# Performance work log

Hardware: AMD Instinct MI355X
Metric: run time of the kernel (lower is better)

Reference implementation:

```python
import jax, jax.numpy as jnp
import numpy as np

N_NODES = 50000
N_EDGES = 300000
D_IN = 256
D_HID = 256


def setup_inputs() -> dict:
    key = jax.random.key(0)
    ks = jax.random.split(key, 9)
    x = jax.random.normal(ks[0], (N_NODES, D_IN), dtype=jnp.float32)
    src = jax.random.randint(ks[1], (N_EDGES,), 0, N_NODES, dtype=jnp.int64)
    dst = jax.random.randint(ks[2], (N_EDGES,), 0, N_NODES, dtype=jnp.int64)
    # Kaiming-uniform-ish init like nn.Linear defaults
    def lin(k, fan_in, fan_out):
        bound = 1.0 / np.sqrt(fan_in)
        kw, kb = jax.random.split(k)
        W = jax.random.uniform(kw, (fan_out, fan_in), minval=-bound, maxval=bound, dtype=jnp.float32)
        b = jax.random.uniform(kb, (fan_out,), minval=-bound, maxval=bound, dtype=jnp.float32)
        return W, b
    W1, b1 = lin(ks[3], 2 * D_IN, D_HID)
    W2, b2 = lin(ks[4], D_HID, D_HID)
    W3, b3 = lin(ks[5], D_HID, 1)
    return {"x": x, "src": src, "dst": dst,
            "W1": W1, "b1": b1, "W2": W2, "b2": b2, "W3": W3, "b3": b3}


def reference(x, src, dst, W1, b1, W2, b2, W3, b3):
    # gather src/dst node features per edge and concat -> [E, 2*D_IN]
    h = jnp.concatenate([x[src], x[dst]], axis=1)
    h = jax.nn.relu(h @ W1.T + b1)          # [E, D_HID]
    h = jax.nn.relu(h @ W2.T + b2)          # dropout is identity in eval mode
    score = h @ W3.T + b3                   # [E, 1]
    return score
```

## Files before the change

kernel.cpp:

```cpp
#include <hip/hip_runtime.h>

typedef short bfx8 __attribute__((ext_vector_type(8)));
typedef float fx4 __attribute__((ext_vector_type(4)));

#define D 256
#define E_TILE 64

__device__ __forceinline__ float b2f(short s) {
  union { unsigned u; float f; } v; v.u = ((unsigned)(unsigned short)s) << 16; return v.f;
}
__device__ __forceinline__ short f2b(float f) {
  union { float f; unsigned u; } v; v.f = f;
  unsigned u = v.u;
  u += 0x7fffu + ((u >> 16) & 1u);
  return (short)(u >> 16);
}
__device__ __forceinline__ float relu(float f) { return f > 0.f ? f : 0.f; }

__global__ void k_prep(const float* __restrict__ W1, const float* __restrict__ W2,
                       unsigned short* __restrict__ B1, unsigned short* __restrict__ W2b) {
  int t = blockIdx.x * 256 + threadIdx.x;
  if (t < 512 * 256) {
    int n = t >> 8, k = t & 255;
    float v = (n < 256) ? W1[n * 512 + k] : W1[(n - 256) * 512 + 256 + k];
    B1[t] = (unsigned short)f2b(v);
  } else if (t < 512 * 256 + 256 * 256) {
    int i = t - 512 * 256;
    W2b[i] = (unsigned short)f2b(W2[i]);
  }
}

__launch_bounds__(256, 2)
__global__ void k_node(const float* __restrict__ x, const unsigned short* __restrict__ B1,
                       unsigned short* __restrict__ PQ, int n_nodes) {
  __shared__ __align__(16) short smA[64 * 40];
  __shared__ __align__(16) short smW[512 * 40];
  short* smT = smW;
  const int tid = threadIdx.x;
  const int wave = tid >> 6, lane = tid & 63;
  const int lr = lane & 15, lg = lane >> 4;
  const int m0 = blockIdx.x * 64;

  fx4 acc[4][8] = {};

#pragma unroll 1
  for (int ks = 0; ks < 8; ++ks) {
    const int k0 = ks * 32;
    {
      int r = tid >> 2, c = (tid & 3) * 8;
      int m = m0 + r;
      bfx8 o;
      if (m < n_nodes) {
        const float* p = x + (size_t)m * 256 + k0 + c;
        float4 v0 = *(const float4*)(p);
        float4 v1 = *(const float4*)(p + 4);
        o[0] = f2b(v0.x); o[1] = f2b(v0.y); o[2] = f2b(v0.z); o[3] = f2b(v0.w);
        o[4] = f2b(v1.x); o[5] = f2b(v1.y); o[6] = f2b(v1.z); o[7] = f2b(v1.w);
      } else {
        o = (bfx8){0,0,0,0,0,0,0,0};
      }
      *(bfx8*)&smA[r * 40 + c] = o;
    }
#pragma unroll
    for (int it = 0; it < 8; ++it) {
      int idx = it * 256 + tid;
      int n = idx >> 2, c = (idx & 3) * 8;
      bfx8 v = *(const bfx8*)(B1 + n * 256 + k0 + c);
      *(bfx8*)&smW[n * 40 + c] = v;
    }
    __syncthreads();
    bfx8 af[4];
#pragma unroll
    for (int mt = 0; mt < 4; ++mt)
      af[mt] = *(const bfx8*)&smA[(mt * 16 + lr) * 40 + lg * 8];
#pragma unroll
    for (int nt = 0; nt < 8; ++nt) {
      int n = wave * 128 + nt * 16 + lr;
      bfx8 bf = *(const bfx8*)&smW[n * 40 + lg * 8];
#pragma unroll
      for (int mt = 0; mt < 4; ++mt)
        acc[mt][nt] = __builtin_amdgcn_mfma_f32_16x16x32_bf16(af[mt], bf, acc[mt][nt], 0, 0, 0);
    }
    __syncthreads();
  }

#pragma unroll
  for (int h = 0; h < 2; ++h) {
#pragma unroll
    for (int mt2 = 0; mt2 < 2; ++mt2) {
      const int mt = 2 * h + mt2;
#pragma unroll
      for (int nt = 0; nt < 8; ++nt)
#pragma unroll
        for (int i = 0; i < 4; ++i) {
          int mrow = mt2 * 16 + lg * 4 + i;
          int n = wave * 128 + nt * 16 + lr;
          smT[mrow * 520 + n] = f2b(acc[mt][nt][i]);
        }
    }
    __syncthreads();
    int r = tid >> 3, cbase = (tid & 7) * 8;
    int m = m0 + h * 32 + r;
    if (m < n_nodes) {
#pragma unroll
      for (int j = 0; j < 8; ++j) {
        int c = cbase + j * 64;
        *(bfx8*)(PQ + (size_t)m * 512 + c) = *(const bfx8*)&smT[r * 520 + c];
      }
    }
    __syncthreads();
  }
}

__launch_bounds__(256, 2)
__global__ void k_edge(const unsigned short* __restrict__ PQ,
                       const int* __restrict__ src, const int* __restrict__ dst,
                       const float* __restrict__ b1, const unsigned short* __restrict__ W2b,
                       const float* __restrict__ b2, const float* __restrict__ W3,
                       const float* __restrict__ b3, float* __restrict__ out,
                       int E, int ntiles) {
  __shared__ __align__(16) short smH[64 * 264];
  __shared__ float smS[4][64];
  __shared__ float smB1[256];
  const int tid = threadIdx.x;
  const int wave = tid >> 6, lane = tid & 63;
  const int lr = lane & 15, lg = lane >> 4;

  if (tid < 256) smB1[tid] = b1[tid];

  bfx8 bw[4][8];
  float b2v[4], w3v[4];
#pragma unroll
  for (int nt = 0; nt < 4; ++nt) {
    int n = wave * 64 + nt * 16 + lr;
    b2v[nt] = b2[n];
    w3v[nt] = W3[n];
#pragma unroll
    for (int ks = 0; ks < 8; ++ks)
      bw[nt][ks] = *(const bfx8*)(W2b + n * 256 + ks * 32 + lg * 8);
  }
  const float b3v = b3[0];
  __syncthreads();

  for (int tile = blockIdx.x; tile < ntiles; tile += gridDim.x) {
    const int base = tile * E_TILE;
    {
      int r = tid >> 2;
      int e = base + r;
      if (e < E) {
        int s = src[e], d = dst[e];
        const unsigned short* ps = PQ + (size_t)s * 512;
        const unsigned short* pd = PQ + (size_t)d * 512 + 256;
#pragma unroll
        for (int it = 0; it < 8; ++it) {
          int c = (tid & 3) * 8 + it * 32;
          bfx8 pv = *(const bfx8*)(ps + c);
          bfx8 qv = *(const bfx8*)(pd + c);
          bfx8 o;
#pragma unroll
          for (int j = 0; j < 8; ++j)
            o[j] = f2b(relu(b2f(pv[j]) + b2f(qv[j]) + smB1[c + j]));
          *(bfx8*)&smH[r * 264 + c] = o;
        }
      } else {
        bfx8 z = (bfx8){0,0,0,0,0,0,0,0};
#pragma unroll
        for (int it = 0; it < 8; ++it) {
          int c = (tid & 3) * 8 + it * 32;
          *(bfx8*)&smH[r * 264 + c] = z;
        }
      }
    }
    __syncthreads();

    fx4 acc[4][4] = {};
#pragma unroll
    for (int ks = 0; ks < 8; ++ks) {
      bfx8 af[4];
#pragma unroll
      for (int mt = 0; mt < 4; ++mt)
        af[mt] = *(const bfx8*)&smH[(mt * 16 + lr) * 264 + ks * 32 + lg * 8];
#pragma unroll
      for (int nt = 0; nt < 4; ++nt)
#pragma unroll
        for (int mt = 0; mt < 4; ++mt)
          acc[mt][nt] = __builtin_amdgcn_mfma_f32_16x16x32_bf16(af[mt], bw[nt][ks], acc[mt][nt], 0, 0, 0);
    }

#pragma unroll
    for (int mt = 0; mt < 4; ++mt)
#pragma unroll
      for (int i = 0; i < 4; ++i) {
        float p = 0.f;
#pragma unroll
        for (int nt = 0; nt < 4; ++nt)
          p += relu(acc[mt][nt][i] + b2v[nt]) * w3v[nt];
        p += __shfl_xor(p, 1);
        p += __shfl_xor(p, 2);
        p += __shfl_xor(p, 4);
        p += __shfl_xor(p, 8);
        if (lr == 0) smS[wave][mt * 16 + lg * 4 + i] = p;
      }
    __syncthreads();
    if (tid < 64) {
      int e = base + tid;
      if (e < E) out[e] = smS[0][tid] + smS[1][tid] + smS[2][tid] + smS[3][tid] + b3v;
    }
    __syncthreads();
  }
}

__global__ void k_fallback(const float* __restrict__ x, const int* __restrict__ src,
                           const int* __restrict__ dst, const float* __restrict__ W1,
                           const float* __restrict__ b1, const float* __restrict__ W2,
                           const float* __restrict__ b2, const float* __restrict__ W3,
                           const float* __restrict__ b3, float* __restrict__ out, int E) {
  __shared__ float smF[4][512];
  __shared__ float smG[4][256];
  int wave = threadIdx.x >> 6, lane = threadIdx.x & 63;
  int e = blockIdx.x * 4 + wave;
  bool valid = e < E;
  int ec = valid ? e : 0;
  int s = src[ec], d = dst[ec];
  for (int j = 0; j < 8; ++j) {
    int k = lane * 8 + j;
    smF[wave][k] = (k < 256) ? x[(size_t)s * 256 + k] : x[(size_t)d * 256 + k - 256];
  }
  __syncthreads();
  for (int t = 0; t < 4; ++t) {
    int n = lane + t * 64;
    float a = b1[n];
    for (int k = 0; k < 512; ++k) a += smF[wave][k] * W1[n * 512 + k];
    smG[wave][n] = relu(a);
  }
  __syncthreads();
  float p = 0.f;
  for (int t = 0; t < 4; ++t) {
    int n = lane + t * 64;
    float a = b2[n];
    for (int k = 0; k < 256; ++k) a += smG[wave][k] * W2[n * 256 + k];
    p += relu(a) * W3[n];
  }
  for (int m = 1; m < 64; m <<= 1) p += __shfl_xor(p, m);
  if (lane == 0 && valid) out[e] = p + b3[0];
}

extern "C" void kernel_launch(void* const* d_in, const int* in_sizes, int n_in,
                              void* d_out, int out_size, void* d_ws, size_t ws_size,
                              hipStream_t stream) {
  const float* x  = (const float*)d_in[0];
  const int*   src = (const int*)d_in[1];
  const int*   dst = (const int*)d_in[2];
  const float* W1 = (const float*)d_in[3];
  const float* b1 = (const float*)d_in[4];
  const float* W2 = (const float*)d_in[5];
  const float* b2 = (const float*)d_in[6];
  const float* W3 = (const float*)d_in[7];
  const float* b3 = (const float*)d_in[8];
  float* out = (float*)d_out;

  const int E = in_sizes[1];
  const int n_nodes = in_sizes[0] / 256;

  const size_t offB1 = 0;
  const size_t offW2 = (size_t)512 * 256 * 2;
  const size_t offPQ = offW2 + (size_t)256 * 256 * 2;
  const size_t need = offPQ + (size_t)n_nodes * 512 * 2;

  if (ws_size >= need) {
    unsigned short* B1  = (unsigned short*)((char*)d_ws + offB1);
    unsigned short* W2b = (unsigned short*)((char*)d_ws + offW2);
    unsigned short* PQ  = (unsigned short*)((char*)d_ws + offPQ);
    k_prep<<<768, 256, 0, stream>>>(W1, W2, B1, W2b);
    k_node<<<(n_nodes + 63) / 64, 256, 0, stream>>>(x, B1, PQ, n_nodes);
    const int ntiles = (E + E_TILE - 1) / E_TILE;
    k_edge<<<1024, 256, 0, stream>>>(PQ, src, dst, b1, W2b, b2, W3, b3, out, E, ntiles);
  } else {
    k_fallback<<<(E + 3) / 4, 256, 0, stream>>>(x, src, dst, W1, b1, W2, b2, W3, b3, out, E);
  }
}
```

Measured before the change: 217.3 us.

## Prefetch next edge tile's gathers into registers and double-buffer shared memory

The edge kernel now issues the PQ gathers for the next tile into registers while the MFMA for the current tile runs, and alternates between two shared-memory H buffers, which removes one barrier per tile. The b1 bias is folded into the node-kernel output so the edge kernel no longer reads it from shared memory. The edge grid is halved to 512 blocks to make room for the extra registers and LDS, which raises register pressure and lowers occupancy. Per-edge bias addition before the bf16 rounding of PQ changes the rounding slightly.

After: 266.3 us. 1.23x slower.

```diff
diff --git a/kernel.cpp b/kernel.cpp
--- a/kernel.cpp
+++ b/kernel.cpp
@@ -32,6 +32,7 @@
 
 __launch_bounds__(256, 2)
 __global__ void k_node(const float* __restrict__ x, const unsigned short* __restrict__ B1,
+                       const float* __restrict__ b1,
                        unsigned short* __restrict__ PQ, int n_nodes) {
   __shared__ __align__(16) short smA[64 * 40];
   __shared__ __align__(16) short smW[512 * 40];
@@ -40,6 +41,13 @@
   const int wave = tid >> 6, lane = tid & 63;
   const int lr = lane & 15, lg = lane >> 4;
   const int m0 = blockIdx.x * 64;
+
+  float b1v[8];
+#pragma unroll
+  for (int nt = 0; nt < 8; ++nt) {
+    int n = wave * 128 + nt * 16 + lr;
+    b1v[nt] = (n < 256) ? b1[n] : 0.f;
+  }
 
   fx4 acc[4][8] = {};
 
@@ -95,7 +103,7 @@
         for (int i = 0; i < 4; ++i) {
           int mrow = mt2 * 16 + lg * 4 + i;
           int n = wave * 128 + nt * 16 + lr;
-          smT[mrow * 520 + n] = f2b(acc[mt][nt][i]);
+          smT[mrow * 520 + n] = f2b(acc[mt][nt][i] + b1v[nt]);
         }
     }
     __syncthreads();
@@ -115,18 +123,16 @@
 __launch_bounds__(256, 2)
 __global__ void k_edge(const unsigned short* __restrict__ PQ,
                        const int* __restrict__ src, const int* __restrict__ dst,
-                       const float* __restrict__ b1, const unsigned short* __restrict__ W2b,
+                       const unsigned short* __restrict__ W2b,
                        const float* __restrict__ b2, const float* __restrict__ W3,
                        const float* __restrict__ b3, float* __restrict__ out,
                        int E, int ntiles) {
-  __shared__ __align__(16) short smH[64 * 264];
+  __shared__ __align__(16) short smH[2 * 64 * 264];
   __shared__ float smS[4][64];
-  __shared__ float smB1[256];
   const int tid = threadIdx.x;
   const int wave = tid >> 6, lane = tid & 63;
   const int lr = lane & 15, lg = lane >> 4;
-
-  if (tid < 256) smB1[tid] = b1[tid];
+  const int G = gridDim.x;
 
   bfx8 bw[4][8];
   float b2v[4], w3v[4];
@@ -140,38 +146,54 @@
       bw[nt][ks] = *(const bfx8*)(W2b + n * 256 + ks * 32 + lg * 8);
   }
   const float b3v = b3[0];
-  __syncthreads();
-
-  for (int tile = blockIdx.x; tile < ntiles; tile += gridDim.x) {
-    const int base = tile * E_TILE;
-    {
-      int r = tid >> 2;
-      int e = base + r;
-      if (e < E) {
-        int s = src[e], d = dst[e];
-        const unsigned short* ps = PQ + (size_t)s * 512;
-        const unsigned short* pd = PQ + (size_t)d * 512 + 256;
-#pragma unroll
-        for (int it = 0; it < 8; ++it) {
-          int c = (tid & 3) * 8 + it * 32;
-          bfx8 pv = *(const bfx8*)(ps + c);
-          bfx8 qv = *(const bfx8*)(pd + c);
-          bfx8 o;
-#pragma unroll
-          for (int j = 0; j < 8; ++j)
-            o[j] = f2b(relu(b2f(pv[j]) + b2f(qv[j]) + smB1[c + j]));
-          *(bfx8*)&smH[r * 264 + c] = o;
-        }
-      } else {
-        bfx8 z = (bfx8){0,0,0,0,0,0,0,0};
-#pragma unroll
-        for (int it = 0; it < 8; ++it) {
-          int c = (tid & 3) * 8 + it * 32;
-          *(bfx8*)&smH[r * 264 + c] = z;
-        }
+
+  const int r = tid >> 2, cb = (tid & 3) * 8;
+  const int t0 = blockIdx.x;
+
+  bfx8 pv[8], qv[8];
+  int sN, dN;
+
+  {
+    int e = t0 * E_TILE + r; if (e >= E) e = 0;
+    int s0 = src[e], d0 = dst[e];
+    const unsigned short* ps = PQ + (size_t)s0 * 512;
+    const unsigned short* pd = PQ + (size_t)d0 * 512 + 256;
+#pragma unroll
+    for (int it = 0; it < 8; ++it) {
+      int c = cb + it * 32;
+      pv[it] = *(const bfx8*)(ps + c);
+      qv[it] = *(const bfx8*)(pd + c);
+    }
+    int e2 = (t0 + G) * E_TILE + r; if (e2 >= E) e2 = 0;
+    sN = src[e2]; dN = dst[e2];
+  }
+
+  int buf = 0;
+  for (int t = t0; t < ntiles; t += G) {
+    short* Hb = &smH[buf * (64 * 264)];
+#pragma unroll
+    for (int it = 0; it < 8; ++it) {
+      int c = cb + it * 32;
+      bfx8 o;
+#pragma unroll
+      for (int j = 0; j < 8; ++j)
+        o[j] = f2b(relu(b2f(pv[it][j]) + b2f(qv[it][j])));
+      *(bfx8*)&Hb[r * 264 + c] = o;
+    }
+    __syncthreads();
+
+    if (t + G < ntiles) {
+      const unsigned short* ps = PQ + (size_t)sN * 512;
+      const unsigned short* pd = PQ + (size_t)dN * 512 + 256;
+#pragma unroll
+      for (int it = 0; it < 8; ++it) {
+        int c = cb + it * 32;
+        pv[it] = *(const bfx8*)(ps + c);
+        qv[it] = *(const bfx8*)(pd + c);
       }
-    }
-    __syncthreads();
+      int e2 = (t + 2 * G) * E_TILE + r; if (e2 >= E) e2 = 0;
+      sN = src[e2]; dN = dst[e2];
+    }
 
     fx4 acc[4][4] = {};
 #pragma unroll
@@ -179,7 +201,7 @@
       bfx8 af[4];
 #pragma unroll
       for (int mt = 0; mt < 4; ++mt)
-        af[mt] = *(const bfx8*)&smH[(mt * 16 + lr) * 264 + ks * 32 + lg * 8];
+        af[mt] = *(const bfx8*)&Hb[(mt * 16 + lr) * 264 + ks * 32 + lg * 8];
 #pragma unroll
       for (int nt = 0; nt < 4; ++nt)
 #pragma unroll
@@ -203,10 +225,10 @@
       }
     __syncthreads();
     if (tid < 64) {
-      int e = base + tid;
+      int e = t * E_TILE + tid;
       if (e < E) out[e] = smS[0][tid] + smS[1][tid] + smS[2][tid] + smS[3][tid] + b3v;
     }
-    __syncthreads();
+    buf ^= 1;
   }
 }
 
@@ -272,9 +294,9 @@
     unsigned short* W2b = (unsigned short*)((char*)d_ws + offW2);
     unsigned short* PQ  = (unsigned short*)((char*)d_ws + offPQ);
     k_prep<<<768, 256, 0, stream>>>(W1, W2, B1, W2b);
-    k_node<<<(n_nodes + 63) / 64, 256, 0, stream>>>(x, B1, PQ, n_nodes);
+    k_node<<<(n_nodes + 63) / 64, 256, 0, stream>>>(x, B1, b1, PQ, n_nodes);
     const int ntiles = (E + E_TILE - 1) / E_TILE;
-    k_edge<<<1024, 256, 0, stream>>>(PQ, src, dst, b1, W2b, b2, W3, b3, out, E, ntiles);
+    k_edge<<<512, 256, 0, stream>>>(PQ, src, dst, W2b, b2, W3, b3, out, E, ntiles);
   } else {
     k_fallback<<<(E + 3) / 4, 256, 0, stream>>>(x, src, dst, W1, b1, W2, b2, W3, b3, out, E);
   }
```

## Make node GEMM persistent with register-resident W1 and fold b1 into P

Applied to the files above, without the earlier changes.

The node-projection kernel becomes persistent: 256 blocks of 512 threads loop over 64-row node tiles. Each wave keeps its slice of the bf16 W1 in registers instead of restaging it through shared memory on every K step, and the full 64x256 x tile is staged once per tile. The b1 bias is now added to the P half when P/Q are written, so the edge kernel no longer loads b1 into shared memory or adds it per element. The edge kernel also drops a trailing barrier and its grid is halved. In exchange the node kernel carries high register pressure at occupancy 1, and the larger tile loop may expose load latency.

Result: faster. 209.5 us (-3.6%).

```diff
diff --git a/kernel.cpp b/kernel.cpp
--- a/kernel.cpp
+++ b/kernel.cpp
@@ -30,103 +30,108 @@
   }
 }
 
-__launch_bounds__(256, 2)
+__launch_bounds__(512, 1)
 __global__ void k_node(const float* __restrict__ x, const unsigned short* __restrict__ B1,
-                       unsigned short* __restrict__ PQ, int n_nodes) {
-  __shared__ __align__(16) short smA[64 * 40];
-  __shared__ __align__(16) short smW[512 * 40];
-  short* smT = smW;
+                       const float* __restrict__ b1,
+                       unsigned short* __restrict__ PQ, int n_nodes, int ntiles) {
+  __shared__ __align__(16) short smA[64 * 264];
+  short* smT = smA;
   const int tid = threadIdx.x;
   const int wave = tid >> 6, lane = tid & 63;
   const int lr = lane & 15, lg = lane >> 4;
-  const int m0 = blockIdx.x * 64;
-
-  fx4 acc[4][8] = {};
-
-#pragma unroll 1
-  for (int ks = 0; ks < 8; ++ks) {
-    const int k0 = ks * 32;
+
+  bfx8 bw[4][8];
+  float b1v[4];
+#pragma unroll
+  for (int nt = 0; nt < 4; ++nt) {
+    int n = wave * 64 + nt * 16 + lr;
+    b1v[nt] = (n < 256) ? b1[n] : 0.f;
+#pragma unroll
+    for (int ks = 0; ks < 8; ++ks)
+      bw[nt][ks] = *(const bfx8*)(B1 + n * 256 + ks * 32 + lg * 8);
+  }
+
+  const int r  = tid >> 3;
+  const int c4 = (tid & 7) * 4;
+  const int rs = tid >> 4;
+  const int cs = (tid & 15) * 8;
+
+  for (int tile = blockIdx.x; tile < ntiles; tile += gridDim.x) {
+    const int m0 = tile * 64;
     {
-      int r = tid >> 2, c = (tid & 3) * 8;
       int m = m0 + r;
-      bfx8 o;
       if (m < n_nodes) {
-        const float* p = x + (size_t)m * 256 + k0 + c;
-        float4 v0 = *(const float4*)(p);
-        float4 v1 = *(const float4*)(p + 4);
-        o[0] = f2b(v0.x); o[1] = f2b(v0.y); o[2] = f2b(v0.z); o[3] = f2b(v0.w);
-        o[4] = f2b(v1.x); o[5] = f2b(v1.y); o[6] = f2b(v1.z); o[7] = f2b(v1.w);
+        const float* p = x + (size_t)m * 256 + c4;
+#pragma unroll
+        for (int j = 0; j < 8; ++j) {
+          float4 v = *(const float4*)(p + j * 32);
+          short4 o = { f2b(v.x), f2b(v.y), f2b(v.z), f2b(v.w) };
+          *(short4*)&smA[r * 264 + c4 + j * 32] = o;
+        }
       } else {
-        o = (bfx8){0,0,0,0,0,0,0,0};
-      }
-      *(bfx8*)&smA[r * 40 + c] = o;
-    }
-#pragma unroll
-    for (int it = 0; it < 8; ++it) {
-      int idx = it * 256 + tid;
-      int n = idx >> 2, c = (idx & 3) * 8;
-      bfx8 v = *(const bfx8*)(B1 + n * 256 + k0 + c);
-      *(bfx8*)&smW[n * 40 + c] = v;
-    }
-    __syncthreads();
-    bfx8 af[4];
-#pragma unroll
-    for (int mt = 0; mt < 4; ++mt)
-      af[mt] = *(const bfx8*)&smA[(mt * 16 + lr) * 40 + lg * 8];
-#pragma unroll
-    for (int nt = 0; nt < 8; ++nt) {
-      int n = wave * 128 + nt * 16 + lr;
-      bfx8 bf = *(const bfx8*)&smW[n * 40 + lg * 8];
+        short4 z = {0, 0, 0, 0};
+#pragma unroll
+        for (int j = 0; j < 8; ++j)
+          *(short4*)&smA[r * 264 + c4 + j * 32] = z;
+      }
+    }
+    __syncthreads();
+
+    fx4 acc[4][4] = {};
+#pragma unroll
+    for (int ks = 0; ks < 8; ++ks) {
+      bfx8 af[4];
 #pragma unroll
       for (int mt = 0; mt < 4; ++mt)
-        acc[mt][nt] = __builtin_amdgcn_mfma_f32_16x16x32_bf16(af[mt], bf, acc[mt][nt], 0, 0, 0);
-    }
-    __syncthreads();
-  }
-
-#pragma unroll
-  for (int h = 0; h < 2; ++h) {
-#pragma unroll
-    for (int mt2 = 0; mt2 < 2; ++mt2) {
-      const int mt = 2 * h + mt2;
-#pragma unroll
-      for (int nt = 0; nt < 8; ++nt)
-#pragma unroll
-        for (int i = 0; i < 4; ++i) {
-          int mrow = mt2 * 16 + lg * 4 + i;
-          int n = wave * 128 + nt * 16 + lr;
-          smT[mrow * 520 + n] = f2b(acc[mt][nt][i]);
-        }
-    }
-    __syncthreads();
-    int r = tid >> 3, cbase = (tid & 7) * 8;
-    int m = m0 + h * 32 + r;
-    if (m < n_nodes) {
-#pragma unroll
-      for (int j = 0; j < 8; ++j) {
-        int c = cbase + j * 64;
-        *(bfx8*)(PQ + (size_t)m * 512 + c) = *(const bfx8*)&smT[r * 520 + c];
-      }
-    }
-    __syncthreads();
+        af[mt] = *(const bfx8*)&smA[(mt * 16 + lr) * 264 + ks * 32 + lg * 8];
+#pragma unroll
+      for (int nt = 0; nt < 4; ++nt)
+#pragma unroll
+        for (int mt = 0; mt < 4; ++mt)
+          acc[mt][nt] = __builtin_amdgcn_mfma_f32_16x16x32_bf16(af[mt], bw[nt][ks], acc[mt][nt], 0, 0, 0);
+    }
+    __syncthreads();
+
+#pragma unroll
+    for (int h = 0; h < 2; ++h) {
+#pragma unroll
+      for (int mt2 = 0; mt2 < 2; ++mt2) {
+        const int mt = 2 * h + mt2;
+#pragma unroll
+        for (int nt = 0; nt < 4; ++nt)
+#pragma unroll
+          for (int i = 0; i < 4; ++i) {
+            int mrow = mt2 * 16 + lg * 4 + i;
+            int n = wave * 64 + nt * 16 + lr;
+            smT[mrow * 520 + n] = f2b(acc[mt][nt][i] + b1v[nt]);
+          }
+      }
+      __syncthreads();
+      int m = m0 + h * 32 + rs;
+      if (m < n_nodes) {
+#pragma unroll
+        for (int j = 0; j < 4; ++j) {
+          int c = cs + j * 128;
+          *(bfx8*)(PQ + (size_t)m * 512 + c) = *(const bfx8*)&smT[rs * 520 + c];
+        }
+      }
+      __syncthreads();
+    }
   }
 }
 
 __launch_bounds__(256, 2)
 __global__ void k_edge(const unsigned short* __restrict__ PQ,
                        const int* __restrict__ src, const int* __restrict__ dst,
-                       const float* __restrict__ b1, const unsigned short* __restrict__ W2b,
+                       const unsigned short* __restrict__ W2b,
                        const float* __restrict__ b2, const float* __restrict__ W3,
                        const float* __restrict__ b3, float* __restrict__ out,
                        int E, int ntiles) {
   __shared__ __align__(16) short smH[64 * 264];
   __shared__ float smS[4][64];
-  __shared__ float smB1[256];
   const int tid = threadIdx.x;
   const int wave = tid >> 6, lane = tid & 63;
   const int lr = lane & 15, lg = lane >> 4;
-
-  if (tid < 256) smB1[tid] = b1[tid];
 
   bfx8 bw[4][8];
   float b2v[4], w3v[4];
@@ -140,7 +145,6 @@
       bw[nt][ks] = *(const bfx8*)(W2b + n * 256 + ks * 32 + lg * 8);
   }
   const float b3v = b3[0];
-  __syncthreads();
 
   for (int tile = blockIdx.x; tile < ntiles; tile += gridDim.x) {
     const int base = tile * E_TILE;
@@ -159,7 +163,7 @@
           bfx8 o;
 #pragma unroll
           for (int j = 0; j < 8; ++j)
-            o[j] = f2b(relu(b2f(pv[j]) + b2f(qv[j]) + smB1[c + j]));
+            o[j] = f2b(relu(b2f(pv[j]) + b2f(qv[j])));
           *(bfx8*)&smH[r * 264 + c] = o;
         }
       } else {
@@ -206,7 +210,6 @@
       int e = base + tid;
       if (e < E) out[e] = smS[0][tid] + smS[1][tid] + smS[2][tid] + smS[3][tid] + b3v;
     }
-    __syncthreads();
   }
 }
 
@@ -272,9 +275,10 @@
     unsigned short* W2b = (unsigned short*)((char*)d_ws + offW2);
     unsigned short* PQ  = (unsigned short*)((char*)d_ws + offPQ);
     k_prep<<<768, 256, 0, stream>>>(W1, W2, B1, W2b);
-    k_node<<<(n_nodes + 63) / 64, 256, 0, stream>>>(x, B1, PQ, n_nodes);
+    const int ntiles_node = (n_nodes + 63) / 64;
+    k_node<<<256, 512, 0, stream>>>(x, B1, b1, PQ, n_nodes, ntiles_node);
     const int ntiles = (E + E_TILE - 1) / E_TILE;
-    k_edge<<<1024, 256, 0, stream>>>(PQ, src, dst, b1, W2b, b2, W3, b3, out, E, ntiles);
+    k_edge<<<512, 256, 0, stream>>>(PQ, src, dst, W2b, b2, W3, b3, out, E, ntiles);
   } else {
     k_fallback<<<(E + 3) / 4, 256, 0, stream>>>(x, src, dst, W1, b1, W2, b2, W3, b3, out, E);
   }
```
